# Performance work log

Measured on AMD Instinct MI355X. Metric: run time of the kernel, lower is better.

## Reference

```python
import jax, jax.numpy as jnp
import numpy as np

# dims: B batch, N spectrum bins, C top-k peaks, K sparse_k, H heads, DH head dim,
# DM hidden, DI role/filler dim (outer_product mode), L layers, S memory slots, OUT classes
B, N, C, K, H, DH, DM, DI, L, S, OUT = 2, 2048, 256, 64, 4, 32, 128, 16, 3, 64, 10


def _gelu(x):
    return jax.nn.gelu(x, approximate=False)  # torch default gelu is exact erf


def _ln(x, g, b, eps=1e-5):
    m = x.mean(-1, keepdims=True)
    v = x.var(-1, keepdims=True)
    return (x - m) / jnp.sqrt(v + eps) * g + b


def setup_inputs() -> dict:
    key = jax.random.key(0)
    ks = iter(jax.random.split(key, 64))
    def p(shape, s=0.05):
        return jax.random.normal(next(ks), shape, jnp.float32) * s
    return {
        "x": jax.random.uniform(next(ks), (B, N), jnp.float32),
        "emb_roles": p((N, DI)),
        "filler_w": p((DI,)),
        "conv_w": p((DI, 1, 5)),
        "conv_b": p((DI,)),
        "outer_w": p((DM, DI * DI)),
        "enc_ng": jnp.ones((DM,), jnp.float32), "enc_nb": jnp.zeros((DM,), jnp.float32),
        "qw": p((L, DM, DM)), "qb": p((L, DM)),
        "kw": p((L, DM, DM)), "kb": p((L, DM)),
        "vw": p((L, DM, DM)), "vb": p((L, DM)),
        "rel_w1": p((L, DH, 3 * DH)), "rel_b1": p((L, DH)),
        "rel_w2": p((L, 1, DH)), "rel_b2": p((L, 1)),
        "ow": p((L, DM, DM)), "ob": p((L, DM)),
        "n1g": jnp.ones((L, DM), jnp.float32), "n1b": jnp.zeros((L, DM), jnp.float32),
        "n2g": jnp.ones((L, DM), jnp.float32), "n2b": jnp.zeros((L, DM), jnp.float32),
        "ffn_w1": p((L, 4 * DM, DM)), "ffn_b1": p((L, 4 * DM)),
        "ffn_w2": p((L, DM, 4 * DM)), "ffn_b2": p((L, DM)),
        "task_query": p((DM,)),
        "slots": p((S, DM)),
        "gru_wih": p((3 * DM, DM)), "gru_whh": p((3 * DM, DM)),
        "gru_bih": p((3 * DM,)), "gru_bhh": p((3 * DM,)),
        "mem_ng": jnp.ones((DM,), jnp.float32), "mem_nb": jnp.zeros((DM,), jnp.float32),
        "head_w": p((OUT, DM)), "head_b": p((OUT,)),
    }


def reference(x, emb_roles, filler_w, conv_w, conv_b, outer_w, enc_ng, enc_nb,
              qw, qb, kw, kb, vw, vb, rel_w1, rel_b1, rel_w2, rel_b2, ow, ob,
              n1g, n1b, n2g, n2b, ffn_w1, ffn_b1, ffn_w2, ffn_b2,
              task_query, slots, gru_wih, gru_whh, gru_bih, gru_bhh,
              mem_ng, mem_nb, head_w, head_b):
    # --- top-k peak selection ---
    x_log = jnp.log1p(jnp.maximum(x, 0.0))
    vals, top_idx = jax.lax.top_k(x_log, C)          # (B,C)
    mz = top_idx.astype(jnp.float32)                  # curr_mz = top_idx.float()
    # --- MultiScaleBindingEncoder ---
    half = DI // 2
    freq = jnp.exp(jnp.arange(half, dtype=jnp.float32) * (-np.log(10000.0) / (half - 1)))
    ang = mz[..., None] * freq                        # (B,C,half)
    roles = jnp.concatenate([jnp.sin(ang), jnp.cos(ang)], -1) + emb_roles[:C][None]  # (B,C,DI)
    f_point = vals[..., None] * filler_w              # Linear(1,DI,no bias)
    xp = jnp.pad(vals, ((0, 0), (2, 2)), mode='reflect')[:, None, :]  # reflection pad k//2
    f_local = jax.lax.conv_general_dilated(xp, conv_w, (1,), 'VALID',
                                           dimension_numbers=('NCW', 'OIW', 'NCW'))
    f_local = _gelu(f_local.transpose(0, 2, 1) + conv_b)
    fillers = _gelu(f_point + f_local)                # (B,C,DI)
    outer = jnp.einsum('bcd,bce->bcde', roles, fillers).reshape(B, C, DI * DI)
    bnd = _ln(outer @ outer_w.T, enc_ng, enc_nb)      # (B,C,DM)
    scale = 1.0 / np.sqrt(DH)
    for i in range(L):
        # --- SparseSecondOrderAttention ---
        q = (bnd @ qw[i].T + qb[i]).reshape(B, C, H, DH).transpose(0, 2, 1, 3)  # (B,H,C,d)
        k = (bnd @ kw[i].T + kb[i]).reshape(B, C, H, DH).transpose(0, 2, 1, 3)
        v = (bnd @ vw[i].T + vb[i]).reshape(B, C, H, DH).transpose(0, 2, 1, 3)
        w1 = rel_w1[i]                                # (d, 3d)
        qp = q @ w1[:, :DH].T
        kp = k @ w1[:, DH:2 * DH].T
        res = qp[:, :, :, None, :] + kp[:, :, None, :, :] + rel_b1[i]           # (B,H,C,C,d)
        res = res + (q[:, :, :, None, :] * k[:, :, None, :, :]) @ w1[:, 2 * DH:].T
        scores = (_gelu(res) @ rel_w2[i].T + rel_b2[i])[..., 0] * scale         # (B,H,C,C)
        minv = jax.lax.top_k(scores, K)[0][..., -1:]  # kth largest per row
        scores = jnp.where(scores >= minv, scores, jnp.float32(-1e9))
        attn = jax.nn.softmax(scores, -1)             # dropout is identity in eval
        out = (attn @ v).transpose(0, 2, 1, 3).reshape(B, C, DM)
        b1 = _ln(bnd + out @ ow[i].T + ob[i], n1g[i], n1b[i])
        ff = _gelu(b1 @ ffn_w1[i].T + ffn_b1[i]) @ ffn_w2[i].T + ffn_b2[i]
        bnd = _ln(b1 + ff, n2g[i], n2b[i])
    # --- TaskQueryReadoutPlus ---
    dms = 1.0 / np.sqrt(DM)
    sc = jnp.einsum('d,bcd->bc', task_query, bnd) * dms
    h = jnp.einsum('bc,bcd->bd', jax.nn.softmax(sc, -1), bnd)
    # --- GatedRelationalMemory ---
    sl = jnp.broadcast_to(slots[None], (B, S, DM))
    sc2 = jnp.einsum('bsd,bcd->bsc', sl, bnd) * dms
    ctx = jnp.einsum('bsc,bcd->bsd', jax.nn.softmax(sc2, -1), bnd)
    gi = ctx @ gru_wih.T + gru_bih
    gh = sl @ gru_whh.T + gru_bhh
    ir, iz, inn = jnp.split(gi, 3, -1)
    hr, hz, hn = jnp.split(gh, 3, -1)
    r = jax.nn.sigmoid(ir + hr)
    z = jax.nn.sigmoid(iz + hz)
    n = jnp.tanh(inn + r * hn)
    mem = _ln(((1.0 - z) * n + z * sl).mean(1), mem_ng, mem_nb)
    return (h + mem) @ head_w.T + head_b
```

## Files before the change

### kernel.cpp

```cpp
#include <hip/hip_runtime.h>
#include <hip/hip_bf16.h>
#include <math.h>

#define Bb 2
#define Nn 2048
#define Cc 256
#define Kk 64
#define Hh 4
#define DHh 32
#define DMm 128
#define DIi 16
#define Ll 3
#define Ss 64
#define OUTn 10

__device__ __forceinline__ float gelu_exact(float x) {
    return 0.5f * x * (1.0f + erff(x * 0.70710678118654752f));
}

__device__ __forceinline__ float dot128_4(const float* a, const float* __restrict__ w) {
    float s0 = 0.f, s1 = 0.f, s2 = 0.f, s3 = 0.f;
#pragma unroll
    for (int e = 0; e < 128; e += 4) {
        s0 = fmaf(a[e],     w[e],     s0);
        s1 = fmaf(a[e + 1], w[e + 1], s1);
        s2 = fmaf(a[e + 2], w[e + 2], s2);
        s3 = fmaf(a[e + 3], w[e + 3], s3);
    }
    return (s0 + s1) + (s2 + s3);
}

template<int NT>
__device__ __forceinline__ float blk_sum(float v, float* red, int t) {
    red[t] = v; __syncthreads();
#pragma unroll
    for (int s = NT >> 1; s > 0; s >>= 1) {
        if (t < s) red[t] += red[t + s];
        __syncthreads();
    }
    float r = red[0];
    __syncthreads();
    return r;
}

template<int NT>
__device__ __forceinline__ float blk_max(float v, float* red, int t) {
    red[t] = v; __syncthreads();
#pragma unroll
    for (int s = NT >> 1; s > 0; s >>= 1) {
        if (t < s) red[t] = fmaxf(red[t], red[t + s]);
        __syncthreads();
    }
    float r = red[0];
    __syncthreads();
    return r;
}

__global__ __launch_bounds__(1024) void k_topk(const float* __restrict__ x,
                                               float* __restrict__ vals,
                                               float* __restrict__ mz) {
    __shared__ float key[Nn];
    __shared__ int   idx[Nn];
    const int b = blockIdx.x, t = threadIdx.x;
    for (int i = t; i < Nn; i += 1024) { key[i] = x[b * Nn + i]; idx[i] = i; }
    __syncthreads();
    for (int k = 2; k <= Nn; k <<= 1) {
        for (int j = k >> 1; j > 0; j >>= 1) {
            for (int i = t; i < Nn; i += 1024) {
                int ixj = i ^ j;
                if (ixj > i) {
                    float va = key[i], vb = key[ixj];
                    int ia = idx[i], ib = idx[ixj];
                    bool aG = (va > vb) || (va == vb && ia < ib);
                    bool desc = ((i & k) == 0);
                    bool dosw = desc ? (!aG) : aG;
                    if (dosw) { key[i] = vb; key[ixj] = va; idx[i] = ib; idx[ixj] = ia; }
                }
            }
            __syncthreads();
        }
    }
    if (t < Cc) {
        vals[b * Cc + t] = log1pf(fmaxf(key[t], 0.f));
        mz[b * Cc + t] = (float)idx[t];
    }
}

__global__ __launch_bounds__(256) void k_encode(const float* __restrict__ vals,
                                                const float* __restrict__ mz,
                                                const float* __restrict__ emb_roles,
                                                const float* __restrict__ filler_w,
                                                const float* __restrict__ conv_w,
                                                const float* __restrict__ conv_b,
                                                const float* __restrict__ outer_w,
                                                const float* __restrict__ g,
                                                const float* __restrict__ bb,
                                                float* __restrict__ bnd) {
    __shared__ float roles[DIi], fill[DIi], outerv[256], ps[2][128], red[256];
    const int bc = blockIdx.x;
    const int b = bc >> 8, c = bc & 255;
    const int t = threadIdx.x;
    const float NEG = -1.3157629102823120f;
    if (t < DIi) {
        float mzv = mz[bc];
        float rr;
        if (t < 8) rr = sinf(mzv * expf((float)t * NEG));
        else       rr = cosf(mzv * expf((float)(t - 8) * NEG));
        roles[t] = rr + emb_roles[c * DIi + t];
    } else if (t < 2 * DIi) {
        int e = t - DIi;
        float vc = vals[bc];
        float fp = vc * filler_w[e];
        float acc = conv_b[e];
#pragma unroll
        for (int kk = 0; kk < 5; ++kk) {
            int pos = c - 2 + kk;
            pos = pos < 0 ? -pos : (pos >= Cc ? 2 * Cc - 2 - pos : pos);
            acc = fmaf(vals[b * Cc + pos], conv_w[e * 5 + kk], acc);
        }
        fill[e] = gelu_exact(fp + gelu_exact(acc));
    }
    __syncthreads();
    outerv[t] = roles[t >> 4] * fill[t & 15];
    __syncthreads();
    const int o = t & 127, seg = t >> 7;
    const float* wrow = outer_w + o * 256 + seg * 128;
    const float* ov = outerv + seg * 128;
    float acc = dot128_4(ov, wrow);
    ps[seg][o] = acc; __syncthreads();
    float t1 = 0.f;
    if (t < 128) t1 = ps[0][t] + ps[1][t];
    float mean = blk_sum<256>(t < 128 ? t1 : 0.f, red, t) * (1.f / 128.f);
    float d0 = t1 - mean;
    float var = blk_sum<256>(t < 128 ? d0 * d0 : 0.f, red, t) * (1.f / 128.f);
    if (t < 128) bnd[bc * DMm + t] = d0 / sqrtf(var + 1e-5f) * g[t] + bb[t];
}

__global__ __launch_bounds__(128) void k_qkv(const float* __restrict__ bnd,
                                             const float* __restrict__ qw, const float* __restrict__ qb,
                                             const float* __restrict__ kw, const float* __restrict__ kb,
                                             const float* __restrict__ vw, const float* __restrict__ vb,
                                             const float* __restrict__ w1,
                                             float* __restrict__ q, float* __restrict__ k,
                                             float* __restrict__ v, float* __restrict__ qp,
                                             float* __restrict__ kp) {
    __shared__ float brow[DMm], prow[DMm];
    const int bid = blockIdx.x;
    const int which = bid >> 9;
    const int bc = bid & 511;
    const int b = bc >> 8, c = bc & 255;
    const int t = threadIdx.x;
    brow[t] = bnd[bc * DMm + t];
    __syncthreads();
    const float* w  = (which == 0) ? qw : (which == 1) ? kw : vw;
    const float* bi = (which == 0) ? qb : (which == 1) ? kb : vb;
    float val = bi[t] + dot128_4(brow, w + t * DMm);
    const int h = t >> 5, d = t & 31;
    const int gi = ((b * Hh + h) * Cc + c) * DHh + d;
    float* outp = (which == 0) ? q : (which == 1) ? k : v;
    outp[gi] = val;
    if (which < 2) {
        prow[t] = val;
        __syncthreads();
        const float* wr = w1 + d * 96 + ((which == 1) ? 32 : 0);
        float acc = 0.f;
#pragma unroll
        for (int e = 0; e < DHh; ++e) acc = fmaf(prow[h * 32 + e], wr[e], acc);
        ((which == 0) ? qp : kp)[gi] = acc;
    }
}

__global__ __launch_bounds__(64) void k_attn(const float* __restrict__ q,
                                             const float* __restrict__ k,
                                             const float* __restrict__ v,
                                             const float* __restrict__ qp,
                                             const float* __restrict__ kp,
                                             const float* __restrict__ w1,
                                             const float* __restrict__ rb1,
                                             const float* __restrict__ w2,
                                             const float* __restrict__ rb2,
                                             float* __restrict__ aout) {
    __shared__ float w3s[DHh * DHh];
    __shared__ float qs[DHh], qps[DHh], rb1s[DHh], w2s[DHh];
    __shared__ float aw[Cc];
    const int bid = blockIdx.x;
    const int t = threadIdx.x;
    const int i = bid & 255, bh = bid >> 8;
    const int rowbase = (bh * Cc + i) * DHh;

#pragma unroll
    for (int m = 0; m < 4; ++m) {
        int f = t + 64 * m;
        int row = f >> 3, c4 = f & 7;
        float4 vv = *reinterpret_cast<const float4*>(w1 + row * 96 + 64 + c4 * 4);
        *reinterpret_cast<float4*>(&w3s[row * 32 + c4 * 4]) = vv;
    }
    if (t < 32) {
        qs[t]   = q[rowbase + t];
        qps[t]  = qp[rowbase + t];
        rb1s[t] = rb1[t];
        w2s[t]  = w2[t];
    }
    __syncthreads();
    const float rb2v = rb2[0];

    float sc4[4];
    for (int r = 0; r < 4; ++r) {
        const int j = r * 64 + t;
        const int jb = (bh * Cc + j) * DHh;
        float kr[32], kpr[32];
        const float4* k4  = reinterpret_cast<const float4*>(k + jb);
        const float4* kp4 = reinterpret_cast<const float4*>(kp + jb);
#pragma unroll
        for (int m = 0; m < 8; ++m) {
            float4 a = k4[m];  kr[4*m] = a.x; kr[4*m+1] = a.y; kr[4*m+2] = a.z; kr[4*m+3] = a.w;
            float4 bq = kp4[m]; kpr[4*m] = bq.x; kpr[4*m+1] = bq.y; kpr[4*m+2] = bq.z; kpr[4*m+3] = bq.w;
        }
        float p[32];
#pragma unroll
        for (int e = 0; e < 32; ++e) p[e] = qs[e] * kr[e];
        float acc = 0.f;
#pragma unroll 4
        for (int d = 0; d < 32; ++d) {
            const float* wr = &w3s[d * 32];
            float r0 = qps[d] + rb1s[d] + kpr[d], r1 = 0.f, r2 = 0.f, r3 = 0.f;
#pragma unroll
            for (int e = 0; e < 8; ++e) {
                r0 = fmaf(p[e],      wr[e],      r0);
                r1 = fmaf(p[8 + e],  wr[8 + e],  r1);
                r2 = fmaf(p[16 + e], wr[16 + e], r2);
                r3 = fmaf(p[24 + e], wr[24 + e], r3);
            }
            float rr = (r0 + r1) + (r2 + r3);
            acc = fmaf(gelu_exact(rr), w2s[d], acc);
        }
        sc4[r] = (acc + rb2v) * 0.17677669529663689f;
    }

    float v0 = sc4[0], v1 = sc4[1], v2 = sc4[2], v3 = sc4[3];
    auto cx_lane = [&](int k_, int j_) {
        float o0 = __shfl_xor(v0, j_), o1 = __shfl_xor(v1, j_);
        float o2 = __shfl_xor(v2, j_), o3 = __shfl_xor(v3, j_);
        bool lower = ((t & j_) == 0);
        bool d0 = (((0 * 64 + t) & k_) == 0);
        bool d1 = (((1 * 64 + t) & k_) == 0);
        bool d2 = (((2 * 64 + t) & k_) == 0);
        bool d3 = (((3 * 64 + t) & k_) == 0);
        v0 = (lower == d0) ? fmaxf(v0, o0) : fminf(v0, o0);
        v1 = (lower == d1) ? fmaxf(v1, o1) : fminf(v1, o1);
        v2 = (lower == d2) ? fmaxf(v2, o2) : fminf(v2, o2);
        v3 = (lower == d3) ? fmaxf(v3, o3) : fminf(v3, o3);
    };
    auto cx_reg1 = [&](int k_) {
        bool dA = (((0 * 64) & k_) == 0);
        bool dB = (((2 * 64) & k_) == 0);
        float aA = v0, bA = v1;
        v0 = dA ? fmaxf(aA, bA) : fminf(aA, bA);
        v1 = dA ? fminf(aA, bA) : fmaxf(aA, bA);
        float aB = v2, bB = v3;
        v2 = dB ? fmaxf(aB, bB) : fminf(aB, bB);
        v3 = dB ? fminf(aB, bB) : fmaxf(aB, bB);
    };
    auto cx_reg2 = [&](int k_) {
        bool dA = (((0 * 64) & k_) == 0);
        bool dB = (((1 * 64) & k_) == 0);
        float aA = v0, bA = v2;
        v0 = dA ? fmaxf(aA, bA) : fminf(aA, bA);
        v2 = dA ? fminf(aA, bA) : fmaxf(aA, bA);
        float aB = v1, bB = v3;
        v1 = dB ? fmaxf(aB, bB) : fminf(aB, bB);
        v3 = dB ? fminf(aB, bB) : fmaxf(aB, bB);
    };
    cx_lane(2, 1);
    cx_lane(4, 2); cx_lane(4, 1);
    cx_lane(8, 4); cx_lane(8, 2); cx_lane(8, 1);
    cx_lane(16, 8); cx_lane(16, 4); cx_lane(16, 2); cx_lane(16, 1);
    cx_lane(32, 16); cx_lane(32, 8); cx_lane(32, 4); cx_lane(32, 2); cx_lane(32, 1);
    cx_lane(64, 32); cx_lane(64, 16); cx_lane(64, 8); cx_lane(64, 4); cx_lane(64, 2); cx_lane(64, 1);
    cx_reg1(128);
    cx_lane(128, 32); cx_lane(128, 16); cx_lane(128, 8); cx_lane(128, 4); cx_lane(128, 2); cx_lane(128, 1);
    cx_reg2(256); cx_reg1(256);
    cx_lane(256, 32); cx_lane(256, 16); cx_lane(256, 8); cx_lane(256, 4); cx_lane(256, 2); cx_lane(256, 1);

    const float minv = __shfl(v0, 63);
    const float mx   = __shfl(v0, 0);

    float ev[4], lsum = 0.f;
#pragma unroll
    for (int r = 0; r < 4; ++r) {
        ev[r] = (sc4[r] >= minv) ? expf(sc4[r] - mx) : 0.f;
        lsum += ev[r];
    }
#pragma unroll
    for (int off = 1; off < 64; off <<= 1) lsum += __shfl_xor(lsum, off);
    const float inv = 1.f / lsum;
#pragma unroll
    for (int r = 0; r < 4; ++r) aw[r * 64 + t] = ev[r] * inv;
    __syncthreads();

    const int d = t & 31, half = t >> 5;
    const float* vb = v + (bh * Cc + half * 128) * DHh + d;
    const float* awh = aw + half * 128;
    float a0 = 0.f, a1 = 0.f, a2 = 0.f, a3 = 0.f;
#pragma unroll 8
    for (int jj = 0; jj < 32; ++jj) {
        a0 = fmaf(awh[jj],      vb[jj * 32],        a0);
        a1 = fmaf(awh[32 + jj], vb[(32 + jj) * 32], a1);
        a2 = fmaf(awh[64 + jj], vb[(64 + jj) * 32], a2);
        a3 = fmaf(awh[96 + jj], vb[(96 + jj) * 32], a3);
    }
    float accv = (a0 + a1) + (a2 + a3);
    accv += __shfl_xor(accv, 32);
    if (t < 32) {
        const int b = bh >> 2, h = bh & 3;
        aout[(b * Cc + i) * DMm + h * DHh + t] = accv;
    }
}

__global__ __launch_bounds__(512) void k_ffn(const float* __restrict__ aout,
                                             const float* __restrict__ ow, const float* __restrict__ ob,
                                             const float* __restrict__ n1g, const float* __restrict__ n1b,
                                             const float* __restrict__ fw1, const float* __restrict__ fb1,
                                             const float* __restrict__ fw2, const float* __restrict__ fb2,
                                             const float* __restrict__ n2g, const float* __restrict__ n2b,
                                             float* __restrict__ bnd) {
    __shared__ float arow[DMm], b1row[DMm], ff1[512], ps[4][128], red[512];
    const int bc = blockIdx.x, t = threadIdx.x;
    if (t < 128) arow[t] = aout[bc * DMm + t];
    __syncthreads();
    const int o = t & 127, seg = t >> 7;
    {
        const float* wr = ow + o * DMm + seg * 32;
        const float* ar = arow + seg * 32;
        float pa = 0.f;
#pragma unroll
        for (int e = 0; e < 32; ++e) pa = fmaf(ar[e], wr[e], pa);
        ps[seg][o] = pa;
    }
    __syncthreads();
    float t1 = 0.f;
    if (t < 128) t1 = bnd[bc * DMm + t] + ob[t] + ((ps[0][t] + ps[1][t]) + (ps[2][t] + ps[3][t]));
    float mean = blk_sum<512>(t < 128 ? t1 : 0.f, red, t) * (1.f / 128.f);
    float d0 = t1 - mean;
    float var = blk_sum<512>(t < 128 ? d0 * d0 : 0.f, red, t) * (1.f / 128.f);
    if (t < 128) b1row[t] = d0 / sqrtf(var + 1e-5f) * n1g[t] + n1b[t];
    __syncthreads();
    ff1[t] = gelu_exact(fb1[t] + dot128_4(b1row, fw1 + t * DMm));
    __syncthreads();
    {
        const float* wr = fw2 + o * 512 + seg * 128;
        const float* fr = ff1 + seg * 128;
        float pb = dot128_4(fr, wr);
        ps[seg][o] = pb;
    }
    __syncthreads();
    float t2 = 0.f;
    if (t < 128) t2 = b1row[t] + fb2[t] + ((ps[0][t] + ps[1][t]) + (ps[2][t] + ps[3][t]));
    mean = blk_sum<512>(t < 128 ? t2 : 0.f, red, t) * (1.f / 128.f);
    d0 = t2 - mean;
    var = blk_sum<512>(t < 128 ? d0 * d0 : 0.f, red, t) * (1.f / 128.f);
    if (t < 128) bnd[bc * DMm + t] = d0 / sqrtf(var + 1e-5f) * n2g[t] + n2b[t];
}

__global__ __launch_bounds__(256) void k_slots(const float* __restrict__ bnd,
                                               const float* __restrict__ slots,
                                               const float* __restrict__ tq,
                                               const float* __restrict__ wih,
                                               const float* __restrict__ whh,
                                               const float* __restrict__ bih,
                                               const float* __restrict__ bhh,
                                               float* __restrict__ contrib,
                                               float* __restrict__ hbuf) {
    __shared__ float sl[DMm], a2[Cc], red[Cc], ctx2[2][128], ctxs[DMm], giS[3 * DMm], ghS[3 * DMm];
    const int bid = blockIdx.x;
    const int b = bid / 65, s = bid % 65;
    const int t = threadIdx.x;
    if (t < DMm) sl[t] = (s < Ss) ? slots[s * DMm + t] : tq[t];
    __syncthreads();
    float sv = dot128_4(sl, bnd + (b * Cc + t) * DMm) * 0.08838834764831845f;
    float mxv = blk_max<256>(sv, red, t);
    float ev = expf(sv - mxv);
    float sum = blk_sum<256>(ev, red, t);
    a2[t] = ev / sum;
    __syncthreads();
    {
        const int o = t & 127, seg = t >> 7;
        float cacc = 0.f;
        for (int cc = 0; cc < 128; ++cc) {
            int c = seg * 128 + cc;
            cacc = fmaf(a2[c], bnd[(b * Cc + c) * DMm + o], cacc);
        }
        ctx2[seg][o] = cacc;
    }
    __syncthreads();
    if (t < DMm) ctxs[t] = ctx2[0][t] + ctx2[1][t];
    __syncthreads();
    if (s == Ss) {
        if (t < DMm) hbuf[b * DMm + t] = ctxs[t];
        return;
    }
    giS[t] = bih[t] + dot128_4(ctxs, wih + t * DMm);
    ghS[t] = bhh[t] + dot128_4(sl, whh + t * DMm);
    if (t < DMm) {
        int o = 256 + t;
        giS[o] = bih[o] + dot128_4(ctxs, wih + o * DMm);
        ghS[o] = bhh[o] + dot128_4(sl, whh + o * DMm);
    }
    __syncthreads();
    if (t < DMm) {
        float r = 1.f / (1.f + expf(-(giS[t] + ghS[t])));
        float z = 1.f / (1.f + expf(-(giS[128 + t] + ghS[128 + t])));
        float n = tanhf(giS[256 + t] + r * ghS[256 + t]);
        contrib[(b * Ss + s) * DMm + t] = (1.f - z) * n + z * sl[t];
    }
}

__global__ __launch_bounds__(128) void k_final(const float* __restrict__ contrib,
                                               const float* __restrict__ hbuf,
                                               const float* __restrict__ mg, const float* __restrict__ mb,
                                               const float* __restrict__ hw, const float* __restrict__ hb,
                                               float* __restrict__ out) {
    __shared__ float hm[DMm], red[128];
    const int b = blockIdx.x, t = threadIdx.x;
    float acc = 0.f;
    for (int s = 0; s < Ss; ++s) acc += contrib[(b * Ss + s) * DMm + t];
    acc *= (1.f / (float)Ss);
    float mean = blk_sum<128>(acc, red, t) * (1.f / 128.f);
    float d0 = acc - mean;
    float var = blk_sum<128>(d0 * d0, red, t) * (1.f / 128.f);
    float memv = d0 / sqrtf(var + 1e-5f) * mg[t] + mb[t];
    hm[t] = hbuf[b * DMm + t] + memv;
    __syncthreads();
    if (t < OUTn) {
        float o = hb[t];
        const float* wr = hw + t * DMm;
#pragma unroll 16
        for (int e = 0; e < DMm; ++e) o = fmaf(hm[e], wr[e], o);
        out[b * OUTn + t] = o;
    }
}

extern "C" void kernel_launch(void* const* d_in, const int* in_sizes, int n_in,
                              void* d_out, int out_size, void* d_ws, size_t ws_size,
                              hipStream_t stream) {
    const float* x         = (const float*)d_in[0];
    const float* emb_roles = (const float*)d_in[1];
    const float* filler_w  = (const float*)d_in[2];
    const float* conv_w    = (const float*)d_in[3];
    const float* conv_b    = (const float*)d_in[4];
    const float* outer_w   = (const float*)d_in[5];
    const float* enc_ng    = (const float*)d_in[6];
    const float* enc_nb    = (const float*)d_in[7];
    const float* qw        = (const float*)d_in[8];
    const float* qb        = (const float*)d_in[9];
    const float* kw        = (const float*)d_in[10];
    const float* kb        = (const float*)d_in[11];
    const float* vw        = (const float*)d_in[12];
    const float* vb        = (const float*)d_in[13];
    const float* rel_w1    = (const float*)d_in[14];
    const float* rel_b1    = (const float*)d_in[15];
    const float* rel_w2    = (const float*)d_in[16];
    const float* rel_b2    = (const float*)d_in[17];
    const float* ow        = (const float*)d_in[18];
    const float* ob        = (const float*)d_in[19];
    const float* n1g       = (const float*)d_in[20];
    const float* n1b       = (const float*)d_in[21];
    const float* n2g       = (const float*)d_in[22];
    const float* n2b       = (const float*)d_in[23];
    const float* ffn_w1    = (const float*)d_in[24];
    const float* ffn_b1    = (const float*)d_in[25];
    const float* ffn_w2    = (const float*)d_in[26];
    const float* ffn_b2    = (const float*)d_in[27];
    const float* task_q    = (const float*)d_in[28];
    const float* slots     = (const float*)d_in[29];
    const float* gru_wih   = (const float*)d_in[30];
    const float* gru_whh   = (const float*)d_in[31];
    const float* gru_bih   = (const float*)d_in[32];
    const float* gru_bhh   = (const float*)d_in[33];
    const float* mem_ng    = (const float*)d_in[34];
    const float* mem_nb    = (const float*)d_in[35];
    const float* head_w    = (const float*)d_in[36];
    const float* head_b    = (const float*)d_in[37];

    float* ws = (float*)d_ws;
    const int BC = Bb * Cc;
    const int BHCD = Bb * Hh * Cc * DHh;
    float* valsb = ws;
    float* mzb   = valsb + BC;
    float* bnd   = mzb + BC;
    float* qB    = bnd + BC * DMm;
    float* kB    = qB + BHCD;
    float* vB    = kB + BHCD;
    float* qpB   = vB + BHCD;
    float* kpB   = qpB + BHCD;
    float* aout  = kpB + BHCD;
    float* hbuf  = aout + BC * DMm;
    float* contrib = hbuf + Bb * DMm;

    k_topk<<<Bb, 1024, 0, stream>>>(x, valsb, mzb);
    k_encode<<<BC, 256, 0, stream>>>(valsb, mzb, emb_roles, filler_w, conv_w, conv_b,
                                     outer_w, enc_ng, enc_nb, bnd);
    for (int l = 0; l < Ll; ++l) {
        k_qkv<<<3 * BC, 128, 0, stream>>>(bnd,
                                          qw + l * DMm * DMm, qb + l * DMm,
                                          kw + l * DMm * DMm, kb + l * DMm,
                                          vw + l * DMm * DMm, vb + l * DMm,
                                          rel_w1 + l * DHh * 3 * DHh,
                                          qB, kB, vB, qpB, kpB);
        k_attn<<<Bb * Hh * Cc, 64, 0, stream>>>(qB, kB, vB, qpB, kpB,
                                                rel_w1 + l * DHh * 3 * DHh,
                                                rel_b1 + l * DHh,
                                                rel_w2 + l * DHh,
                                                rel_b2 + l,
                                                aout);
        k_ffn<<<BC, 512, 0, stream>>>(aout,
                                      ow + l * DMm * DMm, ob + l * DMm,
                                      n1g + l * DMm, n1b + l * DMm,
                                      ffn_w1 + l * 4 * DMm * DMm, ffn_b1 + l * 4 * DMm,
                                      ffn_w2 + l * 4 * DMm * DMm, ffn_b2 + l * DMm,
                                      n2g + l * DMm, n2b + l * DMm,
                                      bnd);
    }
    k_slots<<<Bb * (Ss + 1), 256, 0, stream>>>(bnd, slots, task_q, gru_wih, gru_whh,
                                               gru_bih, gru_bhh, contrib, hbuf);
    k_final<<<Bb, 128, 0, stream>>>(contrib, hbuf, mem_ng, mem_nb, head_w, head_b, (float*)d_out);
}
```

Before: 546.4 us.

## Widen attention blocks to 256 threads and use wave-shuffle reductions for norms

The relational attention kernel now runs 256 threads per query row, so each thread computes one key score instead of four. Scores are staged in shared memory for the single-wave bitonic top-k, and the attn@V product is split over 8 groups with a shared-memory reduction. Separately, the tree-based block reductions in encode, FFN, slots and final are replaced by wave shuffles plus a small cross-wave combine. LayerNorm variance now uses one pass (E[x²]−mean²), which saves a barrier but is slightly less numerically robust.

```diff
diff --git a/kernel.cpp b/kernel.cpp
--- a/kernel.cpp
+++ b/kernel.cpp
@@ -28,32 +28,6 @@
         s3 = fmaf(a[e + 3], w[e + 3], s3);
     }
     return (s0 + s1) + (s2 + s3);
-}
-
-template<int NT>
-__device__ __forceinline__ float blk_sum(float v, float* red, int t) {
-    red[t] = v; __syncthreads();
-#pragma unroll
-    for (int s = NT >> 1; s > 0; s >>= 1) {
-        if (t < s) red[t] += red[t + s];
-        __syncthreads();
-    }
-    float r = red[0];
-    __syncthreads();
-    return r;
-}
-
-template<int NT>
-__device__ __forceinline__ float blk_max(float v, float* red, int t) {
-    red[t] = v; __syncthreads();
-#pragma unroll
-    for (int s = NT >> 1; s > 0; s >>= 1) {
-        if (t < s) red[t] = fmaxf(red[t], red[t + s]);
-        __syncthreads();
-    }
-    float r = red[0];
-    __syncthreads();
-    return r;
 }
 
 __global__ __launch_bounds__(1024) void k_topk(const float* __restrict__ x,
@@ -96,7 +70,8 @@
                                                 const float* __restrict__ g,
                                                 const float* __restrict__ bb,
                                                 float* __restrict__ bnd) {
-    __shared__ float roles[DIi], fill[DIi], outerv[256], ps[2][128], red[256];
+    __shared__ float roles[DIi], fill[DIi], outerv[256], ps[2][128];
+    __shared__ float redA[4], redB[4];
     const int bc = blockIdx.x;
     const int b = bc >> 8, c = bc & 255;
     const int t = threadIdx.x;
@@ -124,16 +99,21 @@
     outerv[t] = roles[t >> 4] * fill[t & 15];
     __syncthreads();
     const int o = t & 127, seg = t >> 7;
-    const float* wrow = outer_w + o * 256 + seg * 128;
-    const float* ov = outerv + seg * 128;
-    float acc = dot128_4(ov, wrow);
-    ps[seg][o] = acc; __syncthreads();
+    float acc = dot128_4(outerv + seg * 128, outer_w + o * 256 + seg * 128);
+    ps[seg][o] = acc;
+    __syncthreads();
     float t1 = 0.f;
     if (t < 128) t1 = ps[0][t] + ps[1][t];
-    float mean = blk_sum<256>(t < 128 ? t1 : 0.f, red, t) * (1.f / 128.f);
-    float d0 = t1 - mean;
-    float var = blk_sum<256>(t < 128 ? d0 * d0 : 0.f, red, t) * (1.f / 128.f);
-    if (t < 128) bnd[bc * DMm + t] = d0 / sqrtf(var + 1e-5f) * g[t] + bb[t];
+    float sa = (t < 128) ? t1 : 0.f, sb = (t < 128) ? t1 * t1 : 0.f;
+#pragma unroll
+    for (int off = 1; off < 64; off <<= 1) { sa += __shfl_xor(sa, off); sb += __shfl_xor(sb, off); }
+    if ((t & 63) == 0) { redA[t >> 6] = sa; redB[t >> 6] = sb; }
+    __syncthreads();
+    float S = (redA[0] + redA[1]) + (redA[2] + redA[3]);
+    float Q = (redB[0] + redB[1]) + (redB[2] + redB[3]);
+    float mean = S * (1.f / 128.f);
+    float var = Q * (1.f / 128.f) - mean * mean;
+    if (t < 128) bnd[bc * DMm + t] = (t1 - mean) / sqrtf(var + 1e-5f) * g[t] + bb[t];
 }
 
 __global__ __launch_bounds__(128) void k_qkv(const float* __restrict__ bnd,
@@ -170,28 +150,27 @@
     }
 }
 
-__global__ __launch_bounds__(64) void k_attn(const float* __restrict__ q,
-                                             const float* __restrict__ k,
-                                             const float* __restrict__ v,
-                                             const float* __restrict__ qp,
-                                             const float* __restrict__ kp,
-                                             const float* __restrict__ w1,
-                                             const float* __restrict__ rb1,
-                                             const float* __restrict__ w2,
-                                             const float* __restrict__ rb2,
-                                             float* __restrict__ aout) {
+__global__ __launch_bounds__(256) void k_attn(const float* __restrict__ q,
+                                              const float* __restrict__ k,
+                                              const float* __restrict__ v,
+                                              const float* __restrict__ qp,
+                                              const float* __restrict__ kp,
+                                              const float* __restrict__ w1,
+                                              const float* __restrict__ rb1,
+                                              const float* __restrict__ w2,
+                                              const float* __restrict__ rb2,
+                                              float* __restrict__ aout) {
     __shared__ float w3s[DHh * DHh];
     __shared__ float qs[DHh], qps[DHh], rb1s[DHh], w2s[DHh];
-    __shared__ float aw[Cc];
+    __shared__ float scL[Cc], aw[Cc], pr[Cc];
     const int bid = blockIdx.x;
     const int t = threadIdx.x;
+    const int lane = t & 63;
     const int i = bid & 255, bh = bid >> 8;
     const int rowbase = (bh * Cc + i) * DHh;
 
-#pragma unroll
-    for (int m = 0; m < 4; ++m) {
-        int f = t + 64 * m;
-        int row = f >> 3, c4 = f & 7;
+    {
+        int row = t >> 3, c4 = t & 7;
         float4 vv = *reinterpret_cast<const float4*>(w1 + row * 96 + 64 + c4 * 4);
         *reinterpret_cast<float4*>(&w3s[row * 32 + c4 * 4]) = vv;
     }
@@ -204,10 +183,9 @@
     __syncthreads();
     const float rb2v = rb2[0];
 
-    float sc4[4];
-    for (int r = 0; r < 4; ++r) {
-        const int j = r * 64 + t;
-        const int jb = (bh * Cc + j) * DHh;
+    float score;
+    {
+        const int jb = (bh * Cc + t) * DHh;
         float kr[32], kpr[32];
         const float4* k4  = reinterpret_cast<const float4*>(k + jb);
         const float4* kp4 = reinterpret_cast<const float4*>(kp + jb);
@@ -234,18 +212,20 @@
             float rr = (r0 + r1) + (r2 + r3);
             acc = fmaf(gelu_exact(rr), w2s[d], acc);
         }
-        sc4[r] = (acc + rb2v) * 0.17677669529663689f;
-    }
-
-    float v0 = sc4[0], v1 = sc4[1], v2 = sc4[2], v3 = sc4[3];
+        score = (acc + rb2v) * 0.17677669529663689f;
+    }
+    scL[t] = score;
+    __syncthreads();
+
+    float v0 = scL[lane], v1 = scL[64 + lane], v2 = scL[128 + lane], v3 = scL[192 + lane];
     auto cx_lane = [&](int k_, int j_) {
         float o0 = __shfl_xor(v0, j_), o1 = __shfl_xor(v1, j_);
         float o2 = __shfl_xor(v2, j_), o3 = __shfl_xor(v3, j_);
-        bool lower = ((t & j_) == 0);
-        bool d0 = (((0 * 64 + t) & k_) == 0);
-        bool d1 = (((1 * 64 + t) & k_) == 0);
-        bool d2 = (((2 * 64 + t) & k_) == 0);
-        bool d3 = (((3 * 64 + t) & k_) == 0);
+        bool lower = ((lane & j_) == 0);
+        bool d0 = (((0 * 64 + lane) & k_) == 0);
+        bool d1 = (((1 * 64 + lane) & k_) == 0);
+        bool d2 = (((2 * 64 + lane) & k_) == 0);
+        bool d3 = (((3 * 64 + lane) & k_) == 0);
         v0 = (lower == d0) ? fmaxf(v0, o0) : fminf(v0, o0);
         v1 = (lower == d1) ? fmaxf(v1, o1) : fminf(v1, o1);
         v2 = (lower == d2) ? fmaxf(v2, o2) : fminf(v2, o2);
@@ -285,35 +265,37 @@
     const float minv = __shfl(v0, 63);
     const float mx   = __shfl(v0, 0);
 
-    float ev[4], lsum = 0.f;
-#pragma unroll
-    for (int r = 0; r < 4; ++r) {
-        ev[r] = (sc4[r] >= minv) ? expf(sc4[r] - mx) : 0.f;
-        lsum += ev[r];
-    }
-#pragma unroll
-    for (int off = 1; off < 64; off <<= 1) lsum += __shfl_xor(lsum, off);
-    const float inv = 1.f / lsum;
-#pragma unroll
-    for (int r = 0; r < 4; ++r) aw[r * 64 + t] = ev[r] * inv;
-    __syncthreads();
-
-    const int d = t & 31, half = t >> 5;
-    const float* vb = v + (bh * Cc + half * 128) * DHh + d;
-    const float* awh = aw + half * 128;
-    float a0 = 0.f, a1 = 0.f, a2 = 0.f, a3 = 0.f;
-#pragma unroll 8
-    for (int jj = 0; jj < 32; ++jj) {
-        a0 = fmaf(awh[jj],      vb[jj * 32],        a0);
-        a1 = fmaf(awh[32 + jj], vb[(32 + jj) * 32], a1);
-        a2 = fmaf(awh[64 + jj], vb[(64 + jj) * 32], a2);
-        a3 = fmaf(awh[96 + jj], vb[(96 + jj) * 32], a3);
-    }
-    float accv = (a0 + a1) + (a2 + a3);
-    accv += __shfl_xor(accv, 32);
+    float ls = 0.f;
+    ls += expf(v0 - mx);
+    ls += (v1 >= minv) ? expf(v1 - mx) : 0.f;
+    ls += (v2 >= minv) ? expf(v2 - mx) : 0.f;
+    ls += (v3 >= minv) ? expf(v3 - mx) : 0.f;
+#pragma unroll
+    for (int off = 1; off < 64; off <<= 1) ls += __shfl_xor(ls, off);
+    const float inv = 1.f / ls;
+
+    aw[t] = (score >= minv) ? expf(score - mx) * inv : 0.f;
+    __syncthreads();
+
+    const int d = t & 31, grp = t >> 5;
+    const float* vbp = v + (bh * Cc + grp * 32) * DHh + d;
+    const float* awg = aw + grp * 32;
+    float a0 = 0.f, a1 = 0.f, a2v = 0.f, a3v = 0.f;
+#pragma unroll
+    for (int jj = 0; jj < 32; jj += 4) {
+        a0  = fmaf(awg[jj],     vbp[jj * 32],       a0);
+        a1  = fmaf(awg[jj + 1], vbp[(jj + 1) * 32], a1);
+        a2v = fmaf(awg[jj + 2], vbp[(jj + 2) * 32], a2v);
+        a3v = fmaf(awg[jj + 3], vbp[(jj + 3) * 32], a3v);
+    }
+    pr[t] = (a0 + a1) + (a2v + a3v);
+    __syncthreads();
     if (t < 32) {
+        float o = pr[t];
+#pragma unroll
+        for (int g2 = 1; g2 < 8; ++g2) o += pr[g2 * 32 + t];
         const int b = bh >> 2, h = bh & 3;
-        aout[(b * Cc + i) * DMm + h * DHh + t] = accv;
+        aout[(b * Cc + i) * DMm + h * DHh + t] = o;
     }
 }
 
@@ -324,7 +306,8 @@
                                              const float* __restrict__ fw2, const float* __restrict__ fb2,
                                              const float* __restrict__ n2g, const float* __restrict__ n2b,
                                              float* __restrict__ bnd) {
-    __shared__ float arow[DMm], b1row[DMm], ff1[512], ps[4][128], red[512];
+    __shared__ float arow[DMm], b1row[DMm], ff1[512], ps[4][128];
+    __shared__ float redA[8], redB[8], redC[8], redD[8];
     const int bc = blockIdx.x, t = threadIdx.x;
     if (t < 128) arow[t] = aout[bc * DMm + t];
     __syncthreads();
@@ -340,26 +323,41 @@
     __syncthreads();
     float t1 = 0.f;
     if (t < 128) t1 = bnd[bc * DMm + t] + ob[t] + ((ps[0][t] + ps[1][t]) + (ps[2][t] + ps[3][t]));
-    float mean = blk_sum<512>(t < 128 ? t1 : 0.f, red, t) * (1.f / 128.f);
-    float d0 = t1 - mean;
-    float var = blk_sum<512>(t < 128 ? d0 * d0 : 0.f, red, t) * (1.f / 128.f);
-    if (t < 128) b1row[t] = d0 / sqrtf(var + 1e-5f) * n1g[t] + n1b[t];
+    float sa = (t < 128) ? t1 : 0.f, sb = (t < 128) ? t1 * t1 : 0.f;
+#pragma unroll
+    for (int off = 1; off < 64; off <<= 1) { sa += __shfl_xor(sa, off); sb += __shfl_xor(sb, off); }
+    if ((t & 63) == 0) { redA[t >> 6] = sa; redB[t >> 6] = sb; }
+    __syncthreads();
+    float S = 0.f, Q = 0.f;
+#pragma unroll
+    for (int r = 0; r < 8; ++r) { S += redA[r]; Q += redB[r]; }
+    float mean = S * (1.f / 128.f);
+    float var = Q * (1.f / 128.f) - mean * mean;
+    float b1v = 0.f;
+    if (t < 128) {
+        b1v = (t1 - mean) / sqrtf(var + 1e-5f) * n1g[t] + n1b[t];
+        b1row[t] = b1v;
+    }
     __syncthreads();
     ff1[t] = gelu_exact(fb1[t] + dot128_4(b1row, fw1 + t * DMm));
     __syncthreads();
     {
-        const float* wr = fw2 + o * 512 + seg * 128;
-        const float* fr = ff1 + seg * 128;
-        float pb = dot128_4(fr, wr);
-        ps[seg][o] = pb;
+        ps[seg][o] = dot128_4(ff1 + seg * 128, fw2 + o * 512 + seg * 128);
     }
     __syncthreads();
     float t2 = 0.f;
-    if (t < 128) t2 = b1row[t] + fb2[t] + ((ps[0][t] + ps[1][t]) + (ps[2][t] + ps[3][t]));
-    mean = blk_sum<512>(t < 128 ? t2 : 0.f, red, t) * (1.f / 128.f);
-    d0 = t2 - mean;
-    var = blk_sum<512>(t < 128 ? d0 * d0 : 0.f, red, t) * (1.f / 128.f);
-    if (t < 128) bnd[bc * DMm + t] = d0 / sqrtf(var + 1e-5f) * n2g[t] + n2b[t];
+    if (t < 128) t2 = b1v + fb2[t] + ((ps[0][t] + ps[1][t]) + (ps[2][t] + ps[3][t]));
+    sa = (t < 128) ? t2 : 0.f; sb = (t < 128) ? t2 * t2 : 0.f;
+#pragma unroll
+    for (int off = 1; off < 64; off <<= 1) { sa += __shfl_xor(sa, off); sb += __shfl_xor(sb, off); }
+    if ((t & 63) == 0) { redC[t >> 6] = sa; redD[t >> 6] = sb; }
+    __syncthreads();
+    S = 0.f; Q = 0.f;
+#pragma unroll
+    for (int r = 0; r < 8; ++r) { S += redC[r]; Q += redD[r]; }
+    mean = S * (1.f / 128.f);
+    var = Q * (1.f / 128.f) - mean * mean;
+    if (t < 128) bnd[bc * DMm + t] = (t2 - mean) / sqrtf(var + 1e-5f) * n2g[t] + n2b[t];
 }
 
 __global__ __launch_bounds__(256) void k_slots(const float* __restrict__ bnd,
@@ -371,16 +369,27 @@
                                                const float* __restrict__ bhh,
                                                float* __restrict__ contrib,
                                                float* __restrict__ hbuf) {
-    __shared__ float sl[DMm], a2[Cc], red[Cc], ctx2[2][128], ctxs[DMm], giS[3 * DMm], ghS[3 * DMm];
+    __shared__ float sl[DMm], a2[Cc], ctx2[2][128], ctxs[DMm], giS[3 * DMm], ghS[3 * DMm];
+    __shared__ float redM[4], redS[4];
     const int bid = blockIdx.x;
     const int b = bid / 65, s = bid % 65;
     const int t = threadIdx.x;
     if (t < DMm) sl[t] = (s < Ss) ? slots[s * DMm + t] : tq[t];
     __syncthreads();
     float sv = dot128_4(sl, bnd + (b * Cc + t) * DMm) * 0.08838834764831845f;
-    float mxv = blk_max<256>(sv, red, t);
+    float m = sv;
+#pragma unroll
+    for (int off = 1; off < 64; off <<= 1) m = fmaxf(m, __shfl_xor(m, off));
+    if ((t & 63) == 0) redM[t >> 6] = m;
+    __syncthreads();
+    float mxv = fmaxf(fmaxf(redM[0], redM[1]), fmaxf(redM[2], redM[3]));
     float ev = expf(sv - mxv);
-    float sum = blk_sum<256>(ev, red, t);
+    float su = ev;
+#pragma unroll
+    for (int off = 1; off < 64; off <<= 1) su += __shfl_xor(su, off);
+    if ((t & 63) == 0) redS[t >> 6] = su;
+    __syncthreads();
+    float sum = (redS[0] + redS[1]) + (redS[2] + redS[3]);
     a2[t] = ev / sum;
     __syncthreads();
     {
@@ -420,15 +429,20 @@
                                                const float* __restrict__ mg, const float* __restrict__ mb,
                                                const float* __restrict__ hw, const float* __restrict__ hb,
                                                float* __restrict__ out) {
-    __shared__ float hm[DMm], red[128];
+    __shared__ float hm[DMm], redA[2], redB[2];
     const int b = blockIdx.x, t = threadIdx.x;
     float acc = 0.f;
     for (int s = 0; s < Ss; ++s) acc += contrib[(b * Ss + s) * DMm + t];
     acc *= (1.f / (float)Ss);
-    float mean = blk_sum<128>(acc, red, t) * (1.f / 128.f);
-    float d0 = acc - mean;
-    float var = blk_sum<128>(d0 * d0, red, t) * (1.f / 128.f);
-    float memv = d0 / sqrtf(var + 1e-5f) * mg[t] + mb[t];
+    float sa = acc, sb = acc * acc;
+#pragma unroll
+    for (int off = 1; off < 64; off <<= 1) { sa += __shfl_xor(sa, off); sb += __shfl_xor(sb, off); }
+    if ((t & 63) == 0) { redA[t >> 6] = sa; redB[t >> 6] = sb; }
+    __syncthreads();
+    float S = redA[0] + redA[1], Q = redB[0] + redB[1];
+    float mean = S * (1.f / 128.f);
+    float var = Q * (1.f / 128.f) - mean * mean;
+    float memv = (acc - mean) / sqrtf(var + 1e-5f) * mg[t] + mb[t];
     hm[t] = hbuf[b * DMm + t] + memv;
     __syncthreads();
     if (t < OUTn) {
@@ -507,12 +521,12 @@
                                           vw + l * DMm * DMm, vb + l * DMm,
                                           rel_w1 + l * DHh * 3 * DHh,
                                           qB, kB, vB, qpB, kpB);
-        k_attn<<<Bb * Hh * Cc, 64, 0, stream>>>(qB, kB, vB, qpB, kpB,
-                                                rel_w1 + l * DHh * 3 * DHh,
-                                                rel_b1 + l * DHh,
-                                                rel_w2 + l * DHh,
-                                                rel_b2 + l,
-                                                aout);
+        k_attn<<<Bb * Hh * Cc, 256, 0, stream>>>(qB, kB, vB, qpB, kpB,
+                                                 rel_w1 + l * DHh * 3 * DHh,
+                                                 rel_b1 + l * DHh,
+                                                 rel_w2 + l * DHh,
+                                                 rel_b2 + l,
+                                                 aout);
         k_ffn<<<BC, 512, 0, stream>>>(aout,
                                       ow + l * DMm * DMm, ob + l * DMm,
                                       n1g + l * DMm, n1b + l * DMm,
```

After: 498.2 us. 1.1x faster.
